# Optimization experiments

Hardware: AMD Instinct MI355X
Metric: run time of the kernel (lower is better)

## Reference

```python
import jax, jax.numpy as jnp
import numpy as np

B, C, S, E = 2, 4, 2048, 512
H, D, WIN = 8, 64, 256


def _local_windowed_attention(q, k, v, window):
    # q,k,v: [B,H,C,S,D]; causal sliding window of size `window` (keys i-window+1..i)
    b, h, c, s, d = q.shape
    nb = s // window  # S must be divisible by window
    qb = q.reshape(b, h, c, nb, window, d)
    pad = jnp.zeros((b, h, c, 1, window, d), q.dtype)
    kb = jnp.concatenate([pad, k.reshape(b, h, c, nb, window, d)], axis=3)
    vb = jnp.concatenate([pad, v.reshape(b, h, c, nb, window, d)], axis=3)
    # each query block attends to [previous block, own block] -> 2*window keys
    k2 = jnp.concatenate([kb[:, :, :, :-1], kb[:, :, :, 1:]], axis=4)  # [b,h,c,nb,2w,d]
    v2 = jnp.concatenate([vb[:, :, :, :-1], vb[:, :, :, 1:]], axis=4)
    j = jnp.arange(nb)
    qpos = j[:, None] * window + jnp.arange(window)[None, :]              # [nb, w]
    kpos = (j[:, None] - 1) * window + jnp.arange(2 * window)[None, :]    # [nb, 2w]
    diff = qpos[:, :, None] - kpos[:, None, :]                            # [nb, w, 2w]
    mask = (diff >= 0) & (diff < window)  # causal + window; also kills the zero-padding block (j=0)
    scale = 1.0 / np.sqrt(d)
    scores = jnp.einsum('bhcnqd,bhcnkd->bhcnqk', qb, k2) * scale
    scores = jnp.where(mask[None, None, None], scores, jnp.asarray(-1e30, scores.dtype))
    attn = jax.nn.softmax(scores, axis=-1)
    ctx = jnp.einsum('bhcnqk,bhcnkd->bhcnqd', attn, v2)
    return ctx.reshape(b, h, c, s, d)


def setup_inputs() -> dict:
    key = jax.random.key(0)
    ks = jax.random.split(key, 8)
    w_scale = np.sqrt(6.0 / (E + E))  # xavier_uniform for square Linear
    def xav(k):
        return jax.random.uniform(k, (E, E), jnp.float32, -w_scale, w_scale)
    return {
        'query': jax.random.normal(ks[0], (B, C, S, E), jnp.float32),
        'key': jax.random.normal(ks[1], (B, C, S, E), jnp.float32),
        'value': jax.random.normal(ks[2], (B, C, S, E), jnp.float32),
        'Wq': xav(ks[3]), 'bq': jnp.zeros((E,), jnp.float32),
        'Wk': xav(ks[4]), 'bk': jnp.zeros((E,), jnp.float32),
        'Wv': xav(ks[5]), 'bv': jnp.zeros((E,), jnp.float32),
        'Wo': xav(ks[6]), 'bo': jnp.zeros((E,), jnp.float32),
    }


def reference(query, key, value, Wq, bq, Wk, bk, Wv, bv, Wo, bo):
    b, c, s, e = query.shape
    q = query @ Wq.T + bq
    k = key @ Wk.T + bk
    v = value @ Wv.T + bv
    # [b,c,s,e] -> [b,h,c,s,d]
    def split_heads(x):
        return x.reshape(b, c, s, H, D).transpose(0, 3, 1, 2, 4)
    ctx = _local_windowed_attention(split_heads(q), split_heads(k), split_heads(v), WIN)
    # [b,h,c,s,d] -> [b,c,s,e]
    ctx = ctx.transpose(0, 2, 3, 1, 4).reshape(b, c, s, e)
    out = ctx @ Wo.T + bo
    return out
```

## Files before the change

### kernel.cpp

```cpp
#include <hip/hip_runtime.h>
#include <hip/hip_bf16.h>


typedef __bf16 bf16x8 __attribute__((ext_vector_type(8)));
typedef float f32x4 __attribute__((ext_vector_type(4)));
typedef unsigned short u16x8 __attribute__((ext_vector_type(8)));
typedef unsigned int u32x2 __attribute__((ext_vector_type(2)));

#define GLDS(gp, lp) __builtin_amdgcn_global_load_lds( \
    (const __attribute__((address_space(1))) void*)(gp), \
    (__attribute__((address_space(3))) void*)(lp), 16, 0, 0)

__device__ __forceinline__ unsigned short f2bf(float f) {
  unsigned u = __float_as_uint(f);
  return (unsigned short)((u + 0x7fffu + ((u >> 16) & 1u)) >> 16);
}

__global__ void convert_all(const float* __restrict__ q, const float* __restrict__ k,
                            const float* __restrict__ v,
                            const float* __restrict__ wq, const float* __restrict__ wk,
                            const float* __restrict__ wv, const float* __restrict__ wo,
                            unsigned short* __restrict__ dq, unsigned short* __restrict__ dk,
                            unsigned short* __restrict__ dv,
                            unsigned short* __restrict__ dwq, unsigned short* __restrict__ dwk,
                            unsigned short* __restrict__ dwv, unsigned short* __restrict__ dwo) {
  int z = blockIdx.z;
  const float* s;
  unsigned short* d;
  long long i;
  if (z < 3) {
    s = z == 0 ? q : z == 1 ? k : v;
    d = z == 0 ? dq : z == 1 ? dk : dv;
    i = ((long long)blockIdx.x * 256 + threadIdx.x) * 8;
  } else {
    int x = blockIdx.x;
    if (x >= 512) return;
    int wi = x >> 7;
    s = wi == 0 ? wq : wi == 1 ? wk : wi == 2 ? wv : wo;
    d = wi == 0 ? dwq : wi == 1 ? dwk : wi == 2 ? dwv : dwo;
    i = ((long long)(x & 127) * 256 + threadIdx.x) * 8;
  }
  f32x4 a = *reinterpret_cast<const f32x4*>(s + i);
  f32x4 b = *reinterpret_cast<const f32x4*>(s + i + 4);
  u16x8 o;
  o[0] = f2bf(a[0]); o[1] = f2bf(a[1]); o[2] = f2bf(a[2]); o[3] = f2bf(a[3]);
  o[4] = f2bf(b[0]); o[5] = f2bf(b[1]); o[6] = f2bf(b[2]); o[7] = f2bf(b[3]);
  *reinterpret_cast<u16x8*>(d + i) = o;
}

__global__ __launch_bounds__(256, 3)
void gemm_qkv(const unsigned short* __restrict__ Xq, const unsigned short* __restrict__ Xk,
              const unsigned short* __restrict__ Xv,
              const unsigned short* __restrict__ wq, const unsigned short* __restrict__ wk,
              const unsigned short* __restrict__ wv,
              const float* __restrict__ bq, const float* __restrict__ bk,
              const float* __restrict__ bv,
              unsigned short* __restrict__ qout, unsigned short* __restrict__ kout,
              unsigned short* __restrict__ vtout) {
  __shared__ char lds_raw[33280];
  const int z = blockIdx.z;
  const unsigned short* A  = z == 0 ? Xq : z == 1 ? Xk : Xv;
  const unsigned short* Bw = z == 0 ? wq : z == 1 ? wk : wv;
  const float* bias        = z == 0 ? bq : z == 1 ? bk : bv;

  unsigned short* Alds = (unsigned short*)lds_raw;
  unsigned short* Blds = (unsigned short*)(lds_raw + 16384);
  const int t = threadIdx.x;
  const int l = t & 63, w = t >> 6;
  const int lrow = l & 15, lk = l >> 4;
  const int rbase = blockIdx.y * 128, cbase = blockIdx.x * 128;
  const int wm = w >> 1, wn = w & 1;
  f32x4 acc[4][4] = {};

  for (int k0 = 0; k0 < 512; k0 += 64) {
    __syncthreads();
#pragma unroll
    for (int i = 0; i < 4; ++i) {
      int byteoff = w * 4096 + i * 1024;
      int row = w * 32 + i * 8 + (l >> 3);
      int chunk = l & 7;
      GLDS(A + (size_t)(rbase + row) * 512 + k0 + chunk * 8, lds_raw + byteoff);
      GLDS(Bw + (size_t)(cbase + row) * 512 + k0 + chunk * 8, lds_raw + 16384 + byteoff);
    }
    __syncthreads();
    bf16x8 af[4][2], bfr[4][2];
#pragma unroll
    for (int mt = 0; mt < 4; ++mt)
#pragma unroll
      for (int ks = 0; ks < 2; ++ks) {
        af[mt][ks]  = *reinterpret_cast<const bf16x8*>(Alds + (wm * 64 + mt * 16 + lrow) * 64 + ks * 32 + lk * 8);
        bfr[mt][ks] = *reinterpret_cast<const bf16x8*>(Blds + (wn * 64 + mt * 16 + lrow) * 64 + ks * 32 + lk * 8);
      }
#pragma unroll
    for (int mt = 0; mt < 4; ++mt)
#pragma unroll
      for (int nt = 0; nt < 4; ++nt) {
        acc[mt][nt] = __builtin_amdgcn_mfma_f32_16x16x32_bf16(af[mt][0], bfr[nt][0], acc[mt][nt], 0, 0, 0);
        acc[mt][nt] = __builtin_amdgcn_mfma_f32_16x16x32_bf16(af[mt][1], bfr[nt][1], acc[mt][nt], 0, 0, 0);
      }
  }

  float bvv[4];
#pragma unroll
  for (int nt = 0; nt < 4; ++nt) bvv[nt] = bias[cbase + wn * 64 + nt * 16 + lrow];

  if (z < 2) {
    unsigned short* out = z == 0 ? qout : kout;
#pragma unroll
    for (int mt = 0; mt < 4; ++mt)
#pragma unroll
      for (int nt = 0; nt < 4; ++nt)
#pragma unroll
        for (int r = 0; r < 4; ++r) {
          int rg = rbase + wm * 64 + mt * 16 + lk * 4 + r;
          int cg = cbase + wn * 64 + nt * 16 + lrow;
          out[(size_t)rg * 512 + cg] = f2bf(acc[mt][nt][r] + bvv[nt]);
        }
  } else {
    __syncthreads();
    unsigned short* tl = (unsigned short*)lds_raw;
#pragma unroll
    for (int mt = 0; mt < 4; ++mt)
#pragma unroll
      for (int nt = 0; nt < 4; ++nt)
#pragma unroll
        for (int r = 0; r < 4; ++r)
          tl[(wm * 64 + mt * 16 + lk * 4 + r) * 130 + wn * 64 + nt * 16 + lrow] =
              f2bf(acc[mt][nt][r] + bvv[nt]);
    __syncthreads();
    const int bc = rbase >> 11;
    const int sb = rbase & 2047;
#pragma unroll
    for (int rnd = 0; rnd < 8; ++rnd) {
      int idx = rnd * 256 + t;
      int el = idx >> 4;
      int ch = idx & 15;
      u16x8 pk;
#pragma unroll
      for (int j2 = 0; j2 < 8; ++j2) pk[j2] = tl[(ch * 8 + j2) * 130 + el];
      int eg = cbase + el;
      int hh = eg >> 6, dd = eg & 63;
      *reinterpret_cast<u16x8*>(vtout + ((size_t)(bc * 8 + hh) * 64 + dd) * 2048 + sb + ch * 8) = pk;
    }
  }
}

__global__ __launch_bounds__(256, 3)
void gemm_out(const unsigned short* __restrict__ A, const unsigned short* __restrict__ Bw,
              const float* __restrict__ bias, float* __restrict__ out) {
  __shared__ char lds_raw[32768];
  unsigned short* Alds = (unsigned short*)lds_raw;
  unsigned short* Blds = (unsigned short*)(lds_raw + 16384);
  const int t = threadIdx.x;
  const int l = t & 63, w = t >> 6;
  const int lrow = l & 15, lk = l >> 4;
  const int rbase = blockIdx.y * 128, cbase = blockIdx.x * 128;
  const int wm = w >> 1, wn = w & 1;
  f32x4 acc[4][4] = {};

  for (int k0 = 0; k0 < 512; k0 += 64) {
    __syncthreads();
#pragma unroll
    for (int i = 0; i < 4; ++i) {
      int byteoff = w * 4096 + i * 1024;
      int row = w * 32 + i * 8 + (l >> 3);
      int chunk = l & 7;
      GLDS(A + (size_t)(rbase + row) * 512 + k0 + chunk * 8, lds_raw + byteoff);
      GLDS(Bw + (size_t)(cbase + row) * 512 + k0 + chunk * 8, lds_raw + 16384 + byteoff);
    }
    __syncthreads();
    bf16x8 af[4][2], bfr[4][2];
#pragma unroll
    for (int mt = 0; mt < 4; ++mt)
#pragma unroll
      for (int ks = 0; ks < 2; ++ks) {
        af[mt][ks]  = *reinterpret_cast<const bf16x8*>(Alds + (wm * 64 + mt * 16 + lrow) * 64 + ks * 32 + lk * 8);
        bfr[mt][ks] = *reinterpret_cast<const bf16x8*>(Blds + (wn * 64 + mt * 16 + lrow) * 64 + ks * 32 + lk * 8);
      }
#pragma unroll
    for (int mt = 0; mt < 4; ++mt)
#pragma unroll
      for (int nt = 0; nt < 4; ++nt) {
        acc[mt][nt] = __builtin_amdgcn_mfma_f32_16x16x32_bf16(af[mt][0], bfr[nt][0], acc[mt][nt], 0, 0, 0);
        acc[mt][nt] = __builtin_amdgcn_mfma_f32_16x16x32_bf16(af[mt][1], bfr[nt][1], acc[mt][nt], 0, 0, 0);
      }
  }

  float bvv[4];
#pragma unroll
  for (int nt = 0; nt < 4; ++nt) bvv[nt] = bias[cbase + wn * 64 + nt * 16 + lrow];
#pragma unroll
  for (int mt = 0; mt < 4; ++mt)
#pragma unroll
    for (int nt = 0; nt < 4; ++nt)
#pragma unroll
      for (int r = 0; r < 4; ++r) {
        int rg = rbase + wm * 64 + mt * 16 + lk * 4 + r;
        int cg = cbase + wn * 64 + nt * 16 + lrow;
        out[(size_t)rg * 512 + cg] = acc[mt][nt][r] + bvv[nt];
      }
}

__global__ __launch_bounds__(256, 4)
void attn_kernel(const unsigned short* __restrict__ qm, const unsigned short* __restrict__ km,
                 const unsigned short* __restrict__ vtm, unsigned short* __restrict__ ctx) {
  __shared__ char lds_raw[40960];
  const int t = threadIdx.x, l = t & 63, w = t >> 6;
  char* Pl = lds_raw + 32768 + w * 2048;
  const int lm = l & 15, g = l >> 4;

  int flat = blockIdx.x;
  int swz = (flat & 7) * 128 + (flat >> 3);
  const int jh = swz & 15, h = (swz >> 4) & 7, bc = swz >> 7;

  const int Qb = jh * 128;
  const int qlo = Qb + w * 32;
  const int h64 = h * 64;
  const size_t bcrow = (size_t)bc * 2048;
  const size_t bch64 = ((size_t)(bc * 8 + h)) * 64;

  const int tlo = (Qb > 255 ? Qb - 255 : 0) >> 6;
  const int thi = (Qb + 127) >> 6;
  const int nt = thi - tlo + 1;
  const int wlo = (qlo > 255 ? qlo - 255 : 0) >> 6;
  const int whi = (qlo + 31) >> 6;

  auto stage = [&](int tt, int buf) {
    char* Kb = lds_raw + buf * 16384;
#pragma unroll
    for (int i = 0; i < 2; ++i) {
      int byteoff = w * 2048 + i * 1024;
      int row = w * 16 + i * 8 + (l >> 3);
      int clog = (l & 7) ^ (row & 7);
      GLDS(km + (bcrow + tt * 64 + row) * 512 + h64 + clog * 8, Kb + byteoff);
      GLDS(vtm + (bch64 + row) * 2048 + tt * 64 + clog * 8, Kb + 8192 + byteoff);
    }
  };

  bf16x8 qf[2][2];
#pragma unroll
  for (int rt = 0; rt < 2; ++rt)
#pragma unroll
    for (int ks = 0; ks < 2; ++ks)
      qf[rt][ks] = *reinterpret_cast<const bf16x8*>(
          qm + (bcrow + qlo + rt * 16 + lm) * 512 + h64 + ks * 32 + g * 8);

  f32x4 oacc[2][4] = {};
  float ls[2] = {0.f, 0.f};

  stage(tlo, 0);
  __syncthreads();

  for (int it = 0; it < nt; ++it) {
    const int tt = tlo + it;
    if (it + 1 < nt) stage(tt + 1, (it + 1) & 1);

    if (tt >= wlo && tt <= whi) {
      char* Kb = lds_raw + (it & 1) * 16384;
      char* Vb = Kb + 8192;

      f32x4 sc[2][4];
      f32x4 zero = {};
#pragma unroll
      for (int kt = 0; kt < 4; ++kt) {
        int krow = kt * 16 + lm;
        const char* kbase = Kb + krow * 128;
        bf16x8 kf0 = *reinterpret_cast<const bf16x8*>(kbase + ((g ^ (krow & 7)) << 4));
        bf16x8 kf1 = *reinterpret_cast<const bf16x8*>(kbase + (((4 + g) ^ (krow & 7)) << 4));
#pragma unroll
        for (int rt = 0; rt < 2; ++rt) {
          f32x4 s0 = __builtin_amdgcn_mfma_f32_16x16x32_bf16(kf0, qf[rt][0], zero, 0, 0, 0);
          sc[rt][kt] = __builtin_amdgcn_mfma_f32_16x16x32_bf16(kf1, qf[rt][1], s0, 0, 0, 0);
        }
      }

      const bool interior = (tt * 64 + 63 <= qlo) && (tt * 64 >= qlo + 31 - 255);
      if (interior) {
#pragma unroll
        for (int rt = 0; rt < 2; ++rt) {
          float acc = 0.f;
#pragma unroll
          for (int kt = 0; kt < 4; ++kt)
#pragma unroll
            for (int r = 0; r < 4; ++r) {
              float pv = __expf(sc[rt][kt][r] * 0.125f);
              sc[rt][kt][r] = pv;
              acc += pv;
            }
          ls[rt] += acc;
        }
      } else {
#pragma unroll
        for (int rt = 0; rt < 2; ++rt) {
          int d0 = qlo + rt * 16 + lm - (tt * 64 + g * 4);
          float acc = 0.f;
#pragma unroll
          for (int kt = 0; kt < 4; ++kt)
#pragma unroll
            for (int r = 0; r < 4; ++r) {
              bool ok = (unsigned)(d0 - (kt * 16 + r)) <= 255u;
              float pv = ok ? __expf(sc[rt][kt][r] * 0.125f) : 0.f;
              sc[rt][kt][r] = pv;
              acc += pv;
            }
          ls[rt] += acc;
        }
      }

#pragma unroll
      for (int ks = 0; ks < 2; ++ks) {
#pragma unroll
        for (int rt = 0; rt < 2; ++rt)
#pragma unroll
          for (int ktl = 0; ktl < 2; ++ktl) {
            int kt = ks * 2 + ktl;
            unsigned u0, u1;
            asm("v_cvt_pk_bf16_f32 %0, %1, %2" : "=v"(u0) : "v"(sc[rt][kt][0]), "v"(sc[rt][kt][1]));
            asm("v_cvt_pk_bf16_f32 %0, %1, %2" : "=v"(u1) : "v"(sc[rt][kt][2]), "v"(sc[rt][kt][3]));
            u32x2 uu; uu[0] = u0; uu[1] = u1;
            *reinterpret_cast<u32x2*>(Pl + (rt * 16 + lm) * 64 + ktl * 32 + g * 8) = uu;
          }
        bf16x8 pa[2];
        pa[0] = *reinterpret_cast<const bf16x8*>(Pl + lm * 64 + g * 16);
        pa[1] = *reinterpret_cast<const bf16x8*>(Pl + (16 + lm) * 64 + g * 16);
        bf16x8 vb[4];
#pragma unroll
        for (int dt = 0; dt < 4; ++dt) {
          int vrow = dt * 16 + lm;
          vb[dt] = *reinterpret_cast<const bf16x8*>(Vb + vrow * 128 + (((ks * 4 + g) ^ (vrow & 7)) << 4));
        }
#pragma unroll
        for (int rt = 0; rt < 2; ++rt)
#pragma unroll
          for (int dt = 0; dt < 4; ++dt)
            oacc[rt][dt] = __builtin_amdgcn_mfma_f32_16x16x32_bf16(pa[rt], vb[dt], oacc[rt][dt], 0, 0, 0);
      }
    }
    __syncthreads();
  }

#pragma unroll
  for (int rt = 0; rt < 2; ++rt) {
    ls[rt] += __shfl_xor(ls[rt], 16, 64);
    ls[rt] += __shfl_xor(ls[rt], 32, 64);
    int cp = 255 - (qlo + rt * 16 + lm);
    if (cp > 0) ls[rt] += (float)cp;
  }

  float* Pf = (float*)Pl;
  Pf[lm] = 1.f / ls[0];
  Pf[16 + lm] = 1.f / ls[1];
  float inv0[2][4];
#pragma unroll
  for (int rt = 0; rt < 2; ++rt)
#pragma unroll
    for (int r = 0; r < 4; ++r)
      inv0[rt][r] = Pf[rt * 16 + g * 4 + r];

#pragma unroll
  for (int rt = 0; rt < 2; ++rt)
#pragma unroll
    for (int dt = 0; dt < 4; ++dt)
#pragma unroll
      for (int r = 0; r < 4; ++r) {
        size_t rg = bcrow + qlo + rt * 16 + g * 4 + r;
        int cg = h64 + dt * 16 + lm;
        ctx[rg * 512 + cg] = f2bf(oacc[rt][dt][r] * inv0[rt][r]);
      }
}

extern "C" void kernel_launch(void* const* d_in, const int* in_sizes, int n_in,
                              void* d_out, int out_size, void* d_ws, size_t ws_size,
                              hipStream_t stream) {
  const float* q_in = (const float*)d_in[0];
  const float* k_in = (const float*)d_in[1];
  const float* v_in = (const float*)d_in[2];
  const float* Wq = (const float*)d_in[3];
  const float* bq = (const float*)d_in[4];
  const float* Wk = (const float*)d_in[5];
  const float* bk = (const float*)d_in[6];
  const float* Wv = (const float*)d_in[7];
  const float* bv = (const float*)d_in[8];
  const float* Wo = (const float*)d_in[9];
  const float* bo = (const float*)d_in[10];

  char* ws = (char*)d_ws;
  const size_t SZ = (size_t)16384 * 512 * 2;
  unsigned short* Xq = (unsigned short*)(ws);
  unsigned short* Xk = (unsigned short*)(ws + SZ);
  unsigned short* Xv = (unsigned short*)(ws + 2 * SZ);
  unsigned short* qb = (unsigned short*)(ws + 3 * SZ);
  unsigned short* kb = (unsigned short*)(ws + 4 * SZ);
  unsigned short* wq_b = (unsigned short*)(ws + 5 * SZ);
  unsigned short* wk_b = wq_b + 262144;
  unsigned short* wv_b = wk_b + 262144;
  unsigned short* wo_b = wv_b + 262144;
  unsigned short* vtb = (unsigned short*)d_out;
  unsigned short* ctx = Xq;

  convert_all<<<dim3(4096, 1, 4), 256, 0, stream>>>(q_in, k_in, v_in, Wq, Wk, Wv, Wo,
                                                    Xq, Xk, Xv, wq_b, wk_b, wv_b, wo_b);
  gemm_qkv<<<dim3(4, 128, 3), 256, 0, stream>>>(Xq, Xk, Xv, wq_b, wk_b, wv_b,
                                                bq, bk, bv, qb, kb, vtb);
  attn_kernel<<<1024, 256, 0, stream>>>(qb, kb, vtb, ctx);
  gemm_out<<<dim3(4, 128), 256, 0, stream>>>(ctx, wo_b, bo, (float*)d_out);
}
```

Baseline: 250.2 us.

## Fuse fp32-to-bf16 activation conversion into QKV GEMM A-tile loading

Removes the separate conversion pass over the q/k/v activations. The QKV GEMM now reads fp32 activations directly into registers, converts them to bf16 and writes them to LDS with an XOR swizzle, and prefetches the next K-slice during compute. Only the weights are still converted by a smaller kernel. This drops a full write and read of the bf16 activation copies, but the GEMM reads twice the bytes for A, and each of the 4 N-blocks redundantly re-converts the same rows.

```diff
diff --git a/kernel.cpp b/kernel.cpp
--- a/kernel.cpp
+++ b/kernel.cpp
@@ -16,30 +16,14 @@
   return (unsigned short)((u + 0x7fffu + ((u >> 16) & 1u)) >> 16);
 }
 
-__global__ void convert_all(const float* __restrict__ q, const float* __restrict__ k,
-                            const float* __restrict__ v,
-                            const float* __restrict__ wq, const float* __restrict__ wk,
-                            const float* __restrict__ wv, const float* __restrict__ wo,
-                            unsigned short* __restrict__ dq, unsigned short* __restrict__ dk,
-                            unsigned short* __restrict__ dv,
-                            unsigned short* __restrict__ dwq, unsigned short* __restrict__ dwk,
-                            unsigned short* __restrict__ dwv, unsigned short* __restrict__ dwo) {
+__global__ void convert_w(const float* __restrict__ wq, const float* __restrict__ wk,
+                          const float* __restrict__ wv, const float* __restrict__ wo,
+                          unsigned short* __restrict__ dwq, unsigned short* __restrict__ dwk,
+                          unsigned short* __restrict__ dwv, unsigned short* __restrict__ dwo) {
   int z = blockIdx.z;
-  const float* s;
-  unsigned short* d;
-  long long i;
-  if (z < 3) {
-    s = z == 0 ? q : z == 1 ? k : v;
-    d = z == 0 ? dq : z == 1 ? dk : dv;
-    i = ((long long)blockIdx.x * 256 + threadIdx.x) * 8;
-  } else {
-    int x = blockIdx.x;
-    if (x >= 512) return;
-    int wi = x >> 7;
-    s = wi == 0 ? wq : wi == 1 ? wk : wi == 2 ? wv : wo;
-    d = wi == 0 ? dwq : wi == 1 ? dwk : wi == 2 ? dwv : dwo;
-    i = ((long long)(x & 127) * 256 + threadIdx.x) * 8;
-  }
+  const float* s = z == 0 ? wq : z == 1 ? wk : z == 2 ? wv : wo;
+  unsigned short* d = z == 0 ? dwq : z == 1 ? dwk : z == 2 ? dwv : dwo;
+  long long i = ((long long)blockIdx.x * 256 + threadIdx.x) * 8;
   f32x4 a = *reinterpret_cast<const f32x4*>(s + i);
   f32x4 b = *reinterpret_cast<const f32x4*>(s + i + 4);
   u16x8 o;
@@ -49,8 +33,8 @@
 }
 
 __global__ __launch_bounds__(256, 3)
-void gemm_qkv(const unsigned short* __restrict__ Xq, const unsigned short* __restrict__ Xk,
-              const unsigned short* __restrict__ Xv,
+void gemm_qkv(const float* __restrict__ Xq, const float* __restrict__ Xk,
+              const float* __restrict__ Xv,
               const unsigned short* __restrict__ wq, const unsigned short* __restrict__ wk,
               const unsigned short* __restrict__ wv,
               const float* __restrict__ bq, const float* __restrict__ bk,
@@ -59,11 +43,10 @@
               unsigned short* __restrict__ vtout) {
   __shared__ char lds_raw[33280];
   const int z = blockIdx.z;
-  const unsigned short* A  = z == 0 ? Xq : z == 1 ? Xk : Xv;
+  const float* Af          = z == 0 ? Xq : z == 1 ? Xk : Xv;
   const unsigned short* Bw = z == 0 ? wq : z == 1 ? wk : wv;
   const float* bias        = z == 0 ? bq : z == 1 ? bk : bv;
 
-  unsigned short* Alds = (unsigned short*)lds_raw;
   unsigned short* Blds = (unsigned short*)(lds_raw + 16384);
   const int t = threadIdx.x;
   const int l = t & 63, w = t >> 6;
@@ -72,24 +55,52 @@
   const int wm = w >> 1, wn = w & 1;
   f32x4 acc[4][4] = {};
 
+  const int row2 = t >> 1;
+  const int kh = (t & 1) * 32;
+  const float* abase = Af + (size_t)(rbase + row2) * 512 + kh;
+  const int wsw = row2 & 7;
+
+  f32x4 ar[8];
+#pragma unroll
+  for (int i = 0; i < 8; ++i) ar[i] = *reinterpret_cast<const f32x4*>(abase + i * 4);
+
   for (int k0 = 0; k0 < 512; k0 += 64) {
     __syncthreads();
+#pragma unroll
+    for (int j = 0; j < 4; ++j) {
+      bf16x8 pk;
+#pragma unroll
+      for (int e = 0; e < 4; ++e) {
+        pk[e] = (__bf16)ar[2 * j][e];
+        pk[4 + e] = (__bf16)ar[2 * j + 1][e];
+      }
+      int chunk = (kh >> 3) + j;
+      *reinterpret_cast<bf16x8*>(lds_raw + row2 * 128 + ((chunk ^ wsw) << 4)) = pk;
+    }
 #pragma unroll
     for (int i = 0; i < 4; ++i) {
       int byteoff = w * 4096 + i * 1024;
-      int row = w * 32 + i * 8 + (l >> 3);
+      int brow = w * 32 + i * 8 + (l >> 3);
       int chunk = l & 7;
-      GLDS(A + (size_t)(rbase + row) * 512 + k0 + chunk * 8, lds_raw + byteoff);
-      GLDS(Bw + (size_t)(cbase + row) * 512 + k0 + chunk * 8, lds_raw + 16384 + byteoff);
-    }
-    __syncthreads();
+      GLDS(Bw + (size_t)(cbase + brow) * 512 + k0 + chunk * 8, lds_raw + 16384 + byteoff);
+    }
+    __syncthreads();
+    if (k0 + 64 < 512) {
+#pragma unroll
+      for (int i = 0; i < 8; ++i)
+        ar[i] = *reinterpret_cast<const f32x4*>(abase + (k0 + 64) + i * 4);
+    }
+
     bf16x8 af[4][2], bfr[4][2];
 #pragma unroll
     for (int mt = 0; mt < 4; ++mt)
 #pragma unroll
       for (int ks = 0; ks < 2; ++ks) {
-        af[mt][ks]  = *reinterpret_cast<const bf16x8*>(Alds + (wm * 64 + mt * 16 + lrow) * 64 + ks * 32 + lk * 8);
-        bfr[mt][ks] = *reinterpret_cast<const bf16x8*>(Blds + (wn * 64 + mt * 16 + lrow) * 64 + ks * 32 + lk * 8);
+        int arow = wm * 64 + mt * 16 + lrow;
+        af[mt][ks] = *reinterpret_cast<const bf16x8*>(
+            lds_raw + arow * 128 + (((ks * 4 + lk) ^ (arow & 7)) << 4));
+        bfr[mt][ks] = *reinterpret_cast<const bf16x8*>(
+            Blds + (wn * 64 + mt * 16 + lrow) * 64 + ks * 32 + lk * 8);
       }
 #pragma unroll
     for (int mt = 0; mt < 4; ++mt)
@@ -386,9 +397,6 @@
 
   char* ws = (char*)d_ws;
   const size_t SZ = (size_t)16384 * 512 * 2;
-  unsigned short* Xq = (unsigned short*)(ws);
-  unsigned short* Xk = (unsigned short*)(ws + SZ);
-  unsigned short* Xv = (unsigned short*)(ws + 2 * SZ);
   unsigned short* qb = (unsigned short*)(ws + 3 * SZ);
   unsigned short* kb = (unsigned short*)(ws + 4 * SZ);
   unsigned short* wq_b = (unsigned short*)(ws + 5 * SZ);
@@ -396,11 +404,10 @@
   unsigned short* wv_b = wk_b + 262144;
   unsigned short* wo_b = wv_b + 262144;
   unsigned short* vtb = (unsigned short*)d_out;
-  unsigned short* ctx = Xq;
-
-  convert_all<<<dim3(4096, 1, 4), 256, 0, stream>>>(q_in, k_in, v_in, Wq, Wk, Wv, Wo,
-                                                    Xq, Xk, Xv, wq_b, wk_b, wv_b, wo_b);
-  gemm_qkv<<<dim3(4, 128, 3), 256, 0, stream>>>(Xq, Xk, Xv, wq_b, wk_b, wv_b,
+  unsigned short* ctx = (unsigned short*)ws;
+
+  convert_w<<<dim3(128, 1, 4), 256, 0, stream>>>(Wq, Wk, Wv, Wo, wq_b, wk_b, wv_b, wo_b);
+  gemm_qkv<<<dim3(4, 128, 3), 256, 0, stream>>>(q_in, k_in, v_in, wq_b, wk_b, wv_b,
                                                 bq, bk, bv, qb, kb, vtb);
   attn_kernel<<<1024, 256, 0, stream>>>(qb, kb, vtb, ctx);
   gemm_out<<<dim3(4, 128), 256, 0, stream>>>(ctx, wo_b, bo, (float*)d_out);
```

After: 264.4 us. 5.6% more time.
